# Kernel tuning notes

Measured on AMD Instinct MI355X. Metric: run time of the kernel, lower is better.

Reference implementation:

```python
import jax, jax.numpy as jnp
import numpy as np
from jax import lax

D_MODEL = 1024
D_STATE = 16
D_CONV = 4
EXPAND = 2
D_INNER = EXPAND * D_MODEL
LN_EPS = 1e-5


def setup_inputs() -> dict:
    key = jax.random.key(0)
    ks = jax.random.split(key, 12)
    B, L = 4, 1024
    s = lambda fan_in: 1.0 / np.sqrt(fan_in)
    inp = {
        "x": jax.random.normal(ks[0], (B, L, D_MODEL), jnp.float32),
        # in_proj: d_model -> 2*d_inner (stored as (in, out))
        "W_in": jax.random.normal(ks[1], (D_MODEL, 2 * D_INNER), jnp.float32) * s(D_MODEL),
        "b_in": jnp.zeros((2 * D_INNER,), jnp.float32),
        # depthwise causal conv1d, kernel (d_inner, 1, d_conv)
        "conv_w": jax.random.normal(ks[2], (D_INNER, 1, D_CONV), jnp.float32) * s(D_CONV),
        "conv_b": jnp.zeros((D_INNER,), jnp.float32),
        # x_proj: d_inner -> 2*d_state
        "W_xp": jax.random.normal(ks[3], (D_INNER, 2 * D_STATE), jnp.float32) * s(D_INNER),
        "b_xp": jnp.zeros((2 * D_STATE,), jnp.float32),
        # dt_proj: d_inner -> d_inner
        "W_dt": jax.random.normal(ks[4], (D_INNER, D_INNER), jnp.float32) * s(D_INNER),
        "b_dt": jnp.zeros((D_INNER,), jnp.float32),
        # A_log = log(arange(1, d_state+1)) repeated over d_inner
        "A_log": jnp.log(jnp.broadcast_to(jnp.arange(1, D_STATE + 1, dtype=jnp.float32), (D_INNER, D_STATE))),
        "D_param": jnp.ones((D_INNER,), jnp.float32),
        # out_proj: d_inner -> d_model
        "W_out": jax.random.normal(ks[5], (D_INNER, D_MODEL), jnp.float32) * s(D_INNER),
        "b_out": jnp.zeros((D_MODEL,), jnp.float32),
        "ln_g": jnp.ones((D_MODEL,), jnp.float32),
        "ln_b": jnp.zeros((D_MODEL,), jnp.float32),
    }
    return inp


def _causal_depthwise_conv(x, w, b):
    # x: (B, d_inner, L); w: (d_inner, 1, d_conv). Left-pad d_conv-1 => causal.
    y = lax.conv_general_dilated(
        x, w, window_strides=(1,), padding=[(D_CONV - 1, 0)],
        dimension_numbers=("NCH", "OIH", "NCH"), feature_group_count=D_INNER)
    return y + b[None, :, None]


def _ssm(x, A, Bm, Cm, dt, D_param):
    # x, dt: (B,L,D)  A: (D,N)  Bm, Cm: (B,L,N)
    A_disc = jnp.exp(dt[..., None] * A)               # (B,L,D,N)
    dBx = (dt * x)[..., None] * Bm[:, :, None, :]     # (B,L,D,N) = dt*B*x_t
    h0 = jnp.zeros(x.shape[:1] + A.shape, x.dtype)    # (B,D,N)

    def step(h, inputs):
        a, bx, c = inputs                              # (B,D,N),(B,D,N),(B,N)
        h = a * h + bx
        y = jnp.einsum("bdn,bn->bd", h, c)
        return h, y

    _, ys = lax.scan(step, h0, (jnp.swapaxes(A_disc, 0, 1),
                                jnp.swapaxes(dBx, 0, 1),
                                jnp.swapaxes(Cm, 0, 1)))
    y = jnp.swapaxes(ys, 0, 1)                         # (B,L,D)
    return y + x * D_param


def reference(x, W_in, b_in, conv_w, conv_b, W_xp, b_xp, W_dt, b_dt,
              A_log, D_param, W_out, b_out, ln_g, ln_b):
    residual = x
    xr = x @ W_in + b_in                               # (B,L,2*d_inner)
    xi, res = jnp.split(xr, 2, axis=-1)
    xi = jax.nn.silu(xi)
    xi = jnp.swapaxes(xi, 1, 2)                        # (B,d_inner,L)
    xi = _causal_depthwise_conv(xi, conv_w, conv_b)
    xi = jnp.swapaxes(xi, 1, 2)
    xi = jax.nn.silu(xi)
    bc = xi @ W_xp + b_xp                              # (B,L,2*d_state)
    Bm, Cm = jnp.split(bc, 2, axis=-1)
    dt = jax.nn.softplus(xi @ W_dt + b_dt)
    A = -jnp.exp(A_log)                                # (d_inner, d_state)
    y = _ssm(xi, A, Bm, Cm, dt, D_param)
    y = y * jax.nn.silu(res)
    out = y @ W_out + b_out
    z = out + residual
    mu = jnp.mean(z, axis=-1, keepdims=True)
    var = jnp.var(z, axis=-1, keepdims=True)
    return (z - mu) * jax.lax.rsqrt(var + LN_EPS) * ln_g + ln_b
```

## Files before the change

kernel.cpp:

```cpp
#include <hip/hip_runtime.h>
#include <math.h>

#define D_MODEL 1024
#define D_INNER 2048
#define D_STATE 16
#define D_CONV  4
#define NCHUNK  8
#define LCHUNK  128

typedef unsigned short u16;
typedef __attribute__((ext_vector_type(8))) short short8;
typedef __attribute__((ext_vector_type(4))) float f32x4;
typedef __attribute__((ext_vector_type(4))) unsigned short u16x4;

__device__ __forceinline__ float silu_f(float x) { return x / (1.f + __expf(-x)); }
__device__ __forceinline__ float softplus_f(float x) {
    return fmaxf(x, 0.f) + log1pf(__expf(-fabsf(x)));
}
__device__ __forceinline__ u16 f2bf(float f) {
    union { float f; unsigned u; } c; c.f = f;
    unsigned r = c.u + 0x7fffu + ((c.u >> 16) & 1u);
    return (u16)(r >> 16);
}
__device__ __forceinline__ float bf2f(u16 v) {
    union { unsigned u; float f; } c; c.u = ((unsigned)v) << 16; return c.f;
}
__device__ __forceinline__ void gload_lds16(const void* g, void* l) {
    __builtin_amdgcn_global_load_lds((const __attribute__((address_space(1))) void*)g,
                                     (__attribute__((address_space(3))) void*)l, 16, 0, 0);
}

__global__ __launch_bounds__(256)
void f32_to_bf16_kernel(const float* __restrict__ in, u16* __restrict__ out, int n4)
{
    const int i = blockIdx.x * 256 + threadIdx.x;
    if (i >= n4) return;
    const float4 v = *(const float4*)&in[(size_t)i * 4];
    u16x4 o; o.x = f2bf(v.x); o.y = f2bf(v.y); o.z = f2bf(v.z); o.w = f2bf(v.w);
    *(u16x4*)&out[(size_t)i * 4] = o;
}

__global__ __launch_bounds__(256)
void transpose_bf16_kernel(const float* __restrict__ W, u16* __restrict__ Wt, int K, int N)
{
    __shared__ float tile[32][33];
    const int tx = threadIdx.x & 31, ty = threadIdx.x >> 5;
    const int n0 = blockIdx.x * 32, k0 = blockIdx.y * 32;
#pragma unroll
    for (int q = 0; q < 4; q++)
        tile[ty + q * 8][tx] = W[(size_t)(k0 + ty + q * 8) * N + n0 + tx];
    __syncthreads();
#pragma unroll
    for (int q = 0; q < 4; q++)
        Wt[(size_t)(n0 + ty + q * 8) * K + k0 + tx] = f2bf(tile[tx][ty + q * 8]);
}

template <int MODE>
__global__ __launch_bounds__(256)
void gemm_mfma(const u16* __restrict__ A, const u16* __restrict__ Bt,
               const float* __restrict__ bias, const float* __restrict__ aux,
               void* __restrict__ out0v, void* __restrict__ out1v,
               int M, int N, int K)
{
    __shared__ __align__(16) short As[3][4096];
    __shared__ __align__(16) short Bs[3][4096];

    const int tid = threadIdx.x;
    const int wid = tid >> 6, lane = tid & 63;
    const int wr = wid >> 1, wc = wid & 1;
    const int row0 = blockIdx.y * 128, col0 = blockIdx.x * 128;

    f32x4 acc[4][4] = {};

    const int c0 = wid * 128 + lane;
    const int c1 = c0 + 64;
    const u16* Abase = A + (size_t)row0 * K;
    const u16* Bbase = Bt + (size_t)col0 * K;

    const int gsl8 = (((lane & 3) ^ ((lane >> 3) & 3)) << 3);

    const int kg = lane >> 4, r16 = lane & 15;
    const int sl8 = ((kg ^ ((r16 >> 1) & 3)) << 3);

#define STAGE(bi, kk) do {                                                                   \
        gload_lds16(Abase + (size_t)(c0 >> 2) * K + (kk) + gsl8, &As[bi][wid * 1024]);       \
        gload_lds16(Abase + (size_t)(c1 >> 2) * K + (kk) + gsl8, &As[bi][wid * 1024 + 512]); \
        gload_lds16(Bbase + (size_t)(c0 >> 2) * K + (kk) + gsl8, &Bs[bi][wid * 1024]);       \
        gload_lds16(Bbase + (size_t)(c1 >> 2) * K + (kk) + gsl8, &Bs[bi][wid * 1024 + 512]); \
    } while (0)

    const int nt = K >> 5;
    STAGE(0, 0);
    STAGE(1, 32);
    int cs = 0;
    for (int t = 0; t < nt; ++t) {
        if (t + 2 < nt) {
            const int ss = (cs + 2 >= 3) ? cs - 1 : cs + 2;
            STAGE(ss, (t + 2) << 5);
            asm volatile("s_waitcnt vmcnt(8)" ::: "memory");
        } else if (t + 1 < nt) {
            asm volatile("s_waitcnt vmcnt(4)" ::: "memory");
        } else {
            asm volatile("s_waitcnt vmcnt(0)" ::: "memory");
        }
        __builtin_amdgcn_s_barrier();

        short8 af[4], bg[4];
#pragma unroll
        for (int i = 0; i < 4; i++) {
            const int r = wr * 64 + i * 16 + r16;
            af[i] = *(const short8*)&As[cs][r * 32 + sl8];
        }
#pragma unroll
        for (int j = 0; j < 4; j++) {
            const int r = wc * 64 + j * 16 + r16;
            bg[j] = *(const short8*)&Bs[cs][r * 32 + sl8];
        }
        __builtin_amdgcn_s_setprio(1);
#pragma unroll
        for (int i = 0; i < 4; i++)
#pragma unroll
            for (int j = 0; j < 4; j++)
                acc[i][j] = __builtin_amdgcn_mfma_f32_16x16x32_bf16(af[i], bg[j], acc[i][j], 0, 0, 0);
        __builtin_amdgcn_s_setprio(0);

        asm volatile("s_waitcnt lgkmcnt(0)" ::: "memory");
        __builtin_amdgcn_s_barrier();
        cs = (cs + 1 >= 3) ? 0 : cs + 1;
    }
#undef STAGE

#pragma unroll
    for (int i = 0; i < 4; i++) {
#pragma unroll
        for (int j = 0; j < 4; j++) {
#pragma unroll
            for (int r = 0; r < 4; r++) {
                const int row = row0 + wr * 64 + i * 16 + kg * 4 + r;
                const int col = col0 + wc * 64 + j * 16 + r16;
                float v = acc[i][j][r] + bias[col];
                if (MODE == 0) {
                    u16* o0 = (u16*)out0v; u16* o1 = (u16*)out1v;
                    if (col < D_INNER) o0[(size_t)row * D_INNER + col] = f2bf(silu_f(v));
                    else               o1[(size_t)row * D_INNER + (col - D_INNER)] = f2bf(v);
                } else if (MODE == 1) {
                    ((float*)out0v)[(size_t)row * N + col] = softplus_f(v);
                } else {
                    ((float*)out0v)[(size_t)row * N + col] = v + aux[(size_t)row * N + col];
                }
            }
        }
    }
}

__global__ __launch_bounds__(256)
void conv_silu_kernel(const u16* __restrict__ xi, const float* __restrict__ w,
                      const float* __restrict__ cb, float* __restrict__ xc,
                      u16* __restrict__ xcb, int total)
{
    const int i = blockIdx.x * 256 + threadIdx.x;
    if (i >= total) return;
    const int d = i & (D_INNER - 1);
    const int l = (i >> 11) & 1023;
    float acc = cb[d];
#pragma unroll
    for (int k = 0; k < D_CONV; k++) {
        const int li = l + k - (D_CONV - 1);
        if (li >= 0) acc = fmaf(w[d * D_CONV + k], bf2f(xi[(size_t)i + (k - (D_CONV - 1)) * D_INNER]), acc);
    }
    const float s = silu_f(acc);
    xc[i] = s;
    xcb[i] = f2bf(s);
}

__global__ __launch_bounds__(256)
void xproj_mfma_kernel(const u16* __restrict__ A, const u16* __restrict__ Wt,
                       const float* __restrict__ bxp, float* __restrict__ bc)
{
    const int wid = threadIdx.x >> 6, lane = threadIdx.x & 63;
    const int kg = lane >> 4, r16 = lane & 15;
    const int tok0 = blockIdx.x * 64 + wid * 16;

    f32x4 acc[2] = {};
#pragma unroll 4
    for (int k0 = 0; k0 < D_INNER; k0 += 32) {
        const short8 a  = *(const short8*)&A[(size_t)(tok0 + r16) * D_INNER + k0 + kg * 8];
        const short8 b0 = *(const short8*)&Wt[(size_t)r16 * D_INNER + k0 + kg * 8];
        const short8 b1 = *(const short8*)&Wt[(size_t)(16 + r16) * D_INNER + k0 + kg * 8];
        acc[0] = __builtin_amdgcn_mfma_f32_16x16x32_bf16(a, b0, acc[0], 0, 0, 0);
        acc[1] = __builtin_amdgcn_mfma_f32_16x16x32_bf16(a, b1, acc[1], 0, 0, 0);
    }
#pragma unroll
    for (int j = 0; j < 2; j++)
#pragma unroll
        for (int r = 0; r < 4; r++) {
            const int token = tok0 + kg * 4 + r;
            const int c = j * 16 + r16;
            bc[(size_t)token * 32 + c] = acc[j][r] + bxp[c];
        }
}

__global__ __launch_bounds__(256)
void ssm_s1_kernel(const float* __restrict__ xc, const float* __restrict__ dt,
                   const float* __restrict__ bc, const float* __restrict__ A_log,
                   float* __restrict__ hend, float* __restrict__ dtsum)
{
    const int tid = threadIdx.x;
    const int ch = tid >> 4, n = tid & 15;
    const int d0 = blockIdx.x * 16;
    const int c = blockIdx.y;
    const int b = blockIdx.z;
    const int d = d0 + ch;

    const float Aln = -__expf(A_log[d * D_STATE + n]);

    __shared__ float sdt[64][16], sdtx[64][16], sB[64][16];

    float h = 0.f, S = 0.f;

    for (int half = 0; half < 2; half++) {
        const int l0 = c * LCHUNK + half * 64;
        __syncthreads();
        {
            const int l = tid >> 2, di = (tid & 3) << 2;
            const size_t g = ((size_t)(b * 1024 + l0 + l)) * D_INNER + d0 + di;
            const float4 dv = *(const float4*)&dt[g];
            const float4 xv = *(const float4*)&xc[g];
            float4 dx;
            dx.x = dv.x * xv.x; dx.y = dv.y * xv.y; dx.z = dv.z * xv.z; dx.w = dv.w * xv.w;
            *(float4*)&sdt[l][di] = dv;
            *(float4*)&sdtx[l][di] = dx;
            *(float4*)&sB[l][di] = *(const float4*)&bc[((size_t)(b * 1024 + l0 + l)) * 32 + di];
        }
        __syncthreads();
#pragma unroll 16
        for (int l = 0; l < 64; l++) {
            const float dtv = sdt[l][ch];
            const float a = __expf(dtv * Aln);
            h = fmaf(a, h, sdtx[l][ch] * sB[l][n]);
            S += dtv;
        }
    }
    hend[((size_t)(b * NCHUNK + c) * D_INNER + d) * D_STATE + n] = h;
    if (n == 0) dtsum[(size_t)(b * NCHUNK + c) * D_INNER + d] = S;
}

__global__ __launch_bounds__(256)
void ssm_s3_kernel(const float* __restrict__ xc, const float* __restrict__ dt,
                   const float* __restrict__ bc, const float* __restrict__ A_log,
                   const float* __restrict__ Dp, const u16* __restrict__ resbf,
                   const float* __restrict__ hend, const float* __restrict__ dtsum,
                   u16* __restrict__ ybf)
{
    const int tid = threadIdx.x;
    const int wid = tid >> 6, lane = tid & 63;
    const int ch4 = lane >> 4, n = lane & 15;
    const int ch = wid * 4 + ch4;
    const int d0 = blockIdx.x * 16;
    const int c = blockIdx.y;
    const int b = blockIdx.z;
    const int d = d0 + ch;

    const float Aln = -__expf(A_log[d * D_STATE + n]);
    const float Dv = Dp[d];

    float h = 0.f;
    for (int cc = 0; cc < c; cc++) {
        const float S = dtsum[(size_t)(b * NCHUNK + cc) * D_INNER + d];
        const float P = __expf(Aln * S);
        h = fmaf(P, h, hend[((size_t)(b * NCHUNK + cc) * D_INNER + d) * D_STATE + n]);
    }

    __shared__ float sdt[64][16], sdtx[64][16], sx[64][16], sres[64][16];
    __shared__ float sbc[64][32];
    __shared__ float pbuf[4 * 16 * 68];

    float* pw = &pbuf[wid * 16 * 68];

    for (int half = 0; half < 2; half++) {
        const int l0 = c * LCHUNK + half * 64;
        __syncthreads();
        {
            const int l = tid >> 2, di = (tid & 3) << 2;
            const size_t g = ((size_t)(b * 1024 + l0 + l)) * D_INNER + d0 + di;
            const float4 dv = *(const float4*)&dt[g];
            const float4 xv = *(const float4*)&xc[g];
            const u16x4 rv = *(const u16x4*)&resbf[g];
            float4 dx;
            dx.x = dv.x * xv.x; dx.y = dv.y * xv.y; dx.z = dv.z * xv.z; dx.w = dv.w * xv.w;
            *(float4*)&sdt[l][di] = dv;
            *(float4*)&sdtx[l][di] = dx;
            *(float4*)&sx[l][di] = xv;
            sres[l][di + 0] = bf2f(rv.x);
            sres[l][di + 1] = bf2f(rv.y);
            sres[l][di + 2] = bf2f(rv.z);
            sres[l][di + 3] = bf2f(rv.w);
            const int r0 = tid >> 3, c4 = (tid & 7) << 2;
            *(float4*)&sbc[r0][c4] = *(const float4*)&bc[((size_t)(b * 1024 + l0 + r0)) * 32 + c4];
            const int r1 = (tid + 256) >> 3;
            *(float4*)&sbc[r1][c4] = *(const float4*)&bc[((size_t)(b * 1024 + l0 + r1)) * 32 + c4];
        }
        __syncthreads();

        for (int l16 = 0; l16 < 4; l16++) {
#pragma unroll
            for (int j = 0; j < 16; j++) {
                const int l = l16 * 16 + j;
                const float dtv = sdt[l][ch];
                const float a = __expf(dtv * Aln);
                h = fmaf(a, h, sdtx[l][ch] * sbc[l][n]);
                pw[j * 68 + ch4 * 16 + n] = h * sbc[l][16 + n];
            }
            __builtin_amdgcn_wave_barrier();
            const float4 q0 = *(const float4*)&pw[n * 68 + ch4 * 16 + 0];
            const float4 q1 = *(const float4*)&pw[n * 68 + ch4 * 16 + 4];
            const float4 q2 = *(const float4*)&pw[n * 68 + ch4 * 16 + 8];
            const float4 q3 = *(const float4*)&pw[n * 68 + ch4 * 16 + 12];
            const float sum = ((q0.x + q0.y) + (q0.z + q0.w)) + ((q1.x + q1.y) + (q1.z + q1.w))
                            + ((q2.x + q2.y) + (q2.z + q2.w)) + ((q3.x + q3.y) + (q3.z + q3.w));
            const int t = l16 * 16 + n;
            const float xv = sx[t][ch];
            const float rv = sres[t][ch];
            const float yv = (sum + xv * Dv) * silu_f(rv);
            ybf[((size_t)(b * 1024 + l0 + t)) * D_INNER + d] = f2bf(yv);
            __builtin_amdgcn_wave_barrier();
        }
    }
}

__global__ __launch_bounds__(256)
void layernorm_kernel(const float* __restrict__ z, const float* __restrict__ g,
                      const float* __restrict__ beta, float* __restrict__ out)
{
    const int row = blockIdx.x;
    const int tid = threadIdx.x;
    const float* zr = z + (size_t)row * D_MODEL;
    const float4 v = *(const float4*)&zr[tid << 2];
    float s = v.x + v.y + v.z + v.w;
    float ss = v.x * v.x + v.y * v.y + v.z * v.z + v.w * v.w;

    __shared__ float sm[256], sq[256];
    sm[tid] = s; sq[tid] = ss;
    __syncthreads();
    for (int off = 128; off > 0; off >>= 1) {
        if (tid < off) { sm[tid] += sm[tid + off]; sq[tid] += sq[tid + off]; }
        __syncthreads();
    }
    const float mean = sm[0] * (1.f / D_MODEL);
    const float var = sq[0] * (1.f / D_MODEL) - mean * mean;
    const float rstd = rsqrtf(var + 1e-5f);

    float4 o;
    o.x = (v.x - mean) * rstd * g[(tid << 2) + 0] + beta[(tid << 2) + 0];
    o.y = (v.y - mean) * rstd * g[(tid << 2) + 1] + beta[(tid << 2) + 1];
    o.z = (v.z - mean) * rstd * g[(tid << 2) + 2] + beta[(tid << 2) + 2];
    o.w = (v.w - mean) * rstd * g[(tid << 2) + 3] + beta[(tid << 2) + 3];
    *(float4*)&out[(size_t)row * D_MODEL + (tid << 2)] = o;
}

extern "C" void kernel_launch(void* const* d_in, const int* in_sizes, int n_in,
                              void* d_out, int out_size, void* d_ws, size_t ws_size,
                              hipStream_t stream)
{
    const float* x      = (const float*)d_in[0];
    const float* W_in   = (const float*)d_in[1];
    const float* b_in   = (const float*)d_in[2];
    const float* conv_w = (const float*)d_in[3];
    const float* conv_b = (const float*)d_in[4];
    const float* W_xp   = (const float*)d_in[5];
    const float* b_xp   = (const float*)d_in[6];
    const float* W_dt   = (const float*)d_in[7];
    const float* b_dt   = (const float*)d_in[8];
    const float* A_log  = (const float*)d_in[9];
    const float* D_par  = (const float*)d_in[10];
    const float* W_out  = (const float*)d_in[11];
    const float* b_out  = (const float*)d_in[12];
    const float* ln_g   = (const float*)d_in[13];
    const float* ln_b   = (const float*)d_in[14];
    float* out = (float*)d_out;

    const int BL = in_sizes[0] / D_MODEL;
    const int Bb = BL / 1024;
    const size_t BLD = (size_t)BL * D_INNER;

    float* ws    = (float*)d_ws;
    float* xcb   = ws;
    float* dtb   = xcb + BLD;
    float* bcbuf = dtb + BLD;
    float* hend  = bcbuf + (size_t)BL * 32;
    float* dtsum = hend + (size_t)Bb * NCHUNK * D_INNER * D_STATE;
    u16*   xibf  = (u16*)(dtsum + (size_t)Bb * NCHUNK * D_INNER);
    u16*   resbf = xibf + BLD;
    u16*   xcbf  = resbf + BLD;
    u16*   xbf   = xcbf + BLD;
    u16*   wxpT  = xbf + (size_t)BL * D_MODEL;
    u16*   wtmp  = wxpT + 32 * D_INNER;
    u16*   ybf   = xibf;
    float* zbuf  = dtb;

    f32_to_bf16_kernel<<<(BL * D_MODEL / 4 + 255) / 256, 256, 0, stream>>>(x, xbf, BL * D_MODEL / 4);

    transpose_bf16_kernel<<<dim3(2 * D_INNER / 32, D_MODEL / 32), 256, 0, stream>>>(W_in, wtmp, D_MODEL, 2 * D_INNER);

    gemm_mfma<0><<<dim3(2 * D_INNER / 128, BL / 128), 256, 0, stream>>>(
        xbf, wtmp, b_in, nullptr, xibf, resbf, BL, 2 * D_INNER, D_MODEL);

    transpose_bf16_kernel<<<dim3(1, D_INNER / 32), 256, 0, stream>>>(W_xp, wxpT, D_INNER, 32);

    conv_silu_kernel<<<(int)(BLD / 256), 256, 0, stream>>>(
        xibf, conv_w, conv_b, xcb, xcbf, (int)BLD);

    xproj_mfma_kernel<<<BL / 64, 256, 0, stream>>>(xcbf, wxpT, b_xp, bcbuf);

    transpose_bf16_kernel<<<dim3(D_INNER / 32, D_INNER / 32), 256, 0, stream>>>(W_dt, wtmp, D_INNER, D_INNER);

    gemm_mfma<1><<<dim3(D_INNER / 128, BL / 128), 256, 0, stream>>>(
        xcbf, wtmp, b_dt, nullptr, dtb, nullptr, BL, D_INNER, D_INNER);

    ssm_s1_kernel<<<dim3(D_INNER / 16, NCHUNK, Bb), 256, 0, stream>>>(
        xcb, dtb, bcbuf, A_log, hend, dtsum);

    ssm_s3_kernel<<<dim3(D_INNER / 16, NCHUNK, Bb), 256, 0, stream>>>(
        xcb, dtb, bcbuf, A_log, D_par, resbf, hend, dtsum, ybf);

    transpose_bf16_kernel<<<dim3(D_MODEL / 32, D_INNER / 32), 256, 0, stream>>>(W_out, wtmp, D_INNER, D_MODEL);

    gemm_mfma<2><<<dim3(D_MODEL / 128, BL / 128), 256, 0, stream>>>(
        ybf, wtmp, b_out, x, zbuf, nullptr, BL, D_MODEL, D_INNER);

    layernorm_kernel<<<BL, 256, 0, stream>>>(zbuf, ln_g, ln_b, out);
}
```

Baseline: 368.2 us.

## Use 256x256 GEMM tiles for in/dt projections and halve SSM chunk length

Adds a 512-thread GEMM kernel with 256x256 output tiles, a K-step of 64 and double-buffered LDS, and uses it for the in_proj and dt_proj GEMMs. The larger tile raises arithmetic intensity and cuts global reloads. It also halves the SSM chunk length to 64 with twice as many chunks, removing the inner half loop and doubling the parallel blocks in the scan kernels. The risks are fewer blocks per GEMM, which hurts occupancy and wave balance, and a longer cross-chunk combine.

```diff
diff --git a/kernel.cpp b/kernel.cpp
--- a/kernel.cpp
+++ b/kernel.cpp
@@ -5,8 +5,8 @@
 #define D_INNER 2048
 #define D_STATE 16
 #define D_CONV  4
-#define NCHUNK  8
-#define LCHUNK  128
+#define NCHUNK  16
+#define LCHUNK  64
 
 typedef unsigned short u16;
 typedef __attribute__((ext_vector_type(8))) short short8;
@@ -56,11 +56,103 @@
 }
 
 template <int MODE>
-__global__ __launch_bounds__(256)
-void gemm_mfma(const u16* __restrict__ A, const u16* __restrict__ Bt,
-               const float* __restrict__ bias, const float* __restrict__ aux,
-               void* __restrict__ out0v, void* __restrict__ out1v,
-               int M, int N, int K)
+__global__ __launch_bounds__(512, 2)
+void gemm_mfma256(const u16* __restrict__ A, const u16* __restrict__ Bt,
+                  const float* __restrict__ bias,
+                  void* __restrict__ out0v, void* __restrict__ out1v,
+                  int M, int N, int K)
+{
+    __shared__ __align__(16) short As[2][256 * 64];
+    __shared__ __align__(16) short Bs[2][256 * 64];
+
+    const int tid = threadIdx.x;
+    const int wid = tid >> 6, lane = tid & 63;
+    const int wr = wid >> 2, wc = wid & 3;
+    const int row0 = blockIdx.y * 256, col0 = blockIdx.x * 256;
+    const int kg = lane >> 4, r16 = lane & 15;
+
+    f32x4 acc[8][4] = {};
+
+    const u16* Abase = A + (size_t)row0 * K;
+    const u16* Bbase = Bt + (size_t)col0 * K;
+
+#define STAGE256(bi, kk) do {                                                   \
+        _Pragma("unroll")                                                       \
+        for (int q = 0; q < 4; q++) {                                           \
+            const int c = (q << 9) + tid;                                       \
+            const int r = c >> 3;                                               \
+            const int ks8 = (((c & 7) ^ (r & 7)) << 3);                         \
+            gload_lds16(Abase + (size_t)r * K + (kk) + ks8,                     \
+                        &As[bi][(((q << 9) + (wid << 6))) << 3]);               \
+            gload_lds16(Bbase + (size_t)r * K + (kk) + ks8,                     \
+                        &Bs[bi][(((q << 9) + (wid << 6))) << 3]);               \
+        }                                                                       \
+    } while (0)
+
+    const int nt = K >> 6;
+    STAGE256(0, 0);
+    asm volatile("s_waitcnt vmcnt(0)" ::: "memory");
+    __builtin_amdgcn_s_barrier();
+
+    int cur = 0;
+    for (int t = 0; t < nt; ++t) {
+        if (t + 1 < nt) STAGE256(cur ^ 1, (t + 1) << 6);
+
+        const int rx = r16 & 7;
+#pragma unroll
+        for (int ks = 0; ks < 2; ks++) {
+            const int sl8 = (((ks << 2) + kg) ^ rx) << 3;
+            short8 af[8], bg[4];
+#pragma unroll
+            for (int i = 0; i < 8; i++) {
+                const int r = wr * 128 + i * 16 + r16;
+                af[i] = *(const short8*)&As[cur][r * 64 + sl8];
+            }
+#pragma unroll
+            for (int j = 0; j < 4; j++) {
+                const int r = wc * 64 + j * 16 + r16;
+                bg[j] = *(const short8*)&Bs[cur][r * 64 + sl8];
+            }
+            __builtin_amdgcn_s_setprio(1);
+#pragma unroll
+            for (int i = 0; i < 8; i++)
+#pragma unroll
+                for (int j = 0; j < 4; j++)
+                    acc[i][j] = __builtin_amdgcn_mfma_f32_16x16x32_bf16(af[i], bg[j], acc[i][j], 0, 0, 0);
+            __builtin_amdgcn_s_setprio(0);
+        }
+
+        asm volatile("s_waitcnt vmcnt(0)" ::: "memory");
+        __builtin_amdgcn_s_barrier();
+        cur ^= 1;
+    }
+#undef STAGE256
+
+#pragma unroll
+    for (int i = 0; i < 8; i++) {
+#pragma unroll
+        for (int j = 0; j < 4; j++) {
+#pragma unroll
+            for (int r = 0; r < 4; r++) {
+                const int row = row0 + wr * 128 + i * 16 + kg * 4 + r;
+                const int col = col0 + wc * 64 + j * 16 + r16;
+                float v = acc[i][j][r] + bias[col];
+                if (MODE == 0) {
+                    u16* o0 = (u16*)out0v; u16* o1 = (u16*)out1v;
+                    if (col < D_INNER) o0[(size_t)row * D_INNER + col] = f2bf(silu_f(v));
+                    else               o1[(size_t)row * D_INNER + (col - D_INNER)] = f2bf(v);
+                } else {
+                    ((float*)out0v)[(size_t)row * N + col] = softplus_f(v);
+                }
+            }
+        }
+    }
+}
+
+__global__ __launch_bounds__(256)
+void gemm_mfma_128(const u16* __restrict__ A, const u16* __restrict__ Bt,
+                   const float* __restrict__ bias, const float* __restrict__ aux,
+                   float* __restrict__ out0, int M, int N, int K)
 {
     __shared__ __align__(16) short As[3][4096];
     __shared__ __align__(16) short Bs[3][4096];
@@ -78,7 +170,6 @@
     const u16* Bbase = Bt + (size_t)col0 * K;
 
     const int gsl8 = (((lane & 3) ^ ((lane >> 3) & 3)) << 3);
-
     const int kg = lane >> 4, r16 = lane & 15;
     const int sl8 = ((kg ^ ((r16 >> 1) & 3)) << 3);
 
@@ -139,15 +230,7 @@
                 const int row = row0 + wr * 64 + i * 16 + kg * 4 + r;
                 const int col = col0 + wc * 64 + j * 16 + r16;
                 float v = acc[i][j][r] + bias[col];
-                if (MODE == 0) {
-                    u16* o0 = (u16*)out0v; u16* o1 = (u16*)out1v;
-                    if (col < D_INNER) o0[(size_t)row * D_INNER + col] = f2bf(silu_f(v));
-                    else               o1[(size_t)row * D_INNER + (col - D_INNER)] = f2bf(v);
-                } else if (MODE == 1) {
-                    ((float*)out0v)[(size_t)row * N + col] = softplus_f(v);
-                } else {
-                    ((float*)out0v)[(size_t)row * N + col] = v + aux[(size_t)row * N + col];
-                }
+                out0[(size_t)row * N + col] = v + aux[(size_t)row * N + col];
             }
         }
     }
@@ -218,28 +301,25 @@
 
     float h = 0.f, S = 0.f;
 
-    for (int half = 0; half < 2; half++) {
-        const int l0 = c * LCHUNK + half * 64;
-        __syncthreads();
-        {
-            const int l = tid >> 2, di = (tid & 3) << 2;
-            const size_t g = ((size_t)(b * 1024 + l0 + l)) * D_INNER + d0 + di;
-            const float4 dv = *(const float4*)&dt[g];
-            const float4 xv = *(const float4*)&xc[g];
-            float4 dx;
-            dx.x = dv.x * xv.x; dx.y = dv.y * xv.y; dx.z = dv.z * xv.z; dx.w = dv.w * xv.w;
-            *(float4*)&sdt[l][di] = dv;
-            *(float4*)&sdtx[l][di] = dx;
-            *(float4*)&sB[l][di] = *(const float4*)&bc[((size_t)(b * 1024 + l0 + l)) * 32 + di];
-        }
-        __syncthreads();
+    const int l0 = c * LCHUNK;
+    {
+        const int l = tid >> 2, di = (tid & 3) << 2;
+        const size_t g = ((size_t)(b * 1024 + l0 + l)) * D_INNER + d0 + di;
+        const float4 dv = *(const float4*)&dt[g];
+        const float4 xv = *(const float4*)&xc[g];
+        float4 dx;
+        dx.x = dv.x * xv.x; dx.y = dv.y * xv.y; dx.z = dv.z * xv.z; dx.w = dv.w * xv.w;
+        *(float4*)&sdt[l][di] = dv;
+        *(float4*)&sdtx[l][di] = dx;
+        *(float4*)&sB[l][di] = *(const float4*)&bc[((size_t)(b * 1024 + l0 + l)) * 32 + di];
+    }
+    __syncthreads();
 #pragma unroll 16
-        for (int l = 0; l < 64; l++) {
-            const float dtv = sdt[l][ch];
-            const float a = __expf(dtv * Aln);
-            h = fmaf(a, h, sdtx[l][ch] * sB[l][n]);
-            S += dtv;
-        }
+    for (int l = 0; l < 64; l++) {
+        const float dtv = sdt[l][ch];
+        const float a = __expf(dtv * Aln);
+        h = fmaf(a, h, sdtx[l][ch] * sB[l][n]);
+        S += dtv;
     }
     hend[((size_t)(b * NCHUNK + c) * D_INNER + d) * D_STATE + n] = h;
     if (n == 0) dtsum[(size_t)(b * NCHUNK + c) * D_INNER + d] = S;
@@ -277,54 +357,51 @@
 
     float* pw = &pbuf[wid * 16 * 68];
 
-    for (int half = 0; half < 2; half++) {
-        const int l0 = c * LCHUNK + half * 64;
-        __syncthreads();
-        {
-            const int l = tid >> 2, di = (tid & 3) << 2;
-            const size_t g = ((size_t)(b * 1024 + l0 + l)) * D_INNER + d0 + di;
-            const float4 dv = *(const float4*)&dt[g];
-            const float4 xv = *(const float4*)&xc[g];
-            const u16x4 rv = *(const u16x4*)&resbf[g];
-            float4 dx;
-            dx.x = dv.x * xv.x; dx.y = dv.y * xv.y; dx.z = dv.z * xv.z; dx.w = dv.w * xv.w;
-            *(float4*)&sdt[l][di] = dv;
-            *(float4*)&sdtx[l][di] = dx;
-            *(float4*)&sx[l][di] = xv;
-            sres[l][di + 0] = bf2f(rv.x);
-            sres[l][di + 1] = bf2f(rv.y);
-            sres[l][di + 2] = bf2f(rv.z);
-            sres[l][di + 3] = bf2f(rv.w);
-            const int r0 = tid >> 3, c4 = (tid & 7) << 2;
-            *(float4*)&sbc[r0][c4] = *(const float4*)&bc[((size_t)(b * 1024 + l0 + r0)) * 32 + c4];
-            const int r1 = (tid + 256) >> 3;
-            *(float4*)&sbc[r1][c4] = *(const float4*)&bc[((size_t)(b * 1024 + l0 + r1)) * 32 + c4];
-        }
-        __syncthreads();
-
-        for (int l16 = 0; l16 < 4; l16++) {
-#pragma unroll
-            for (int j = 0; j < 16; j++) {
-                const int l = l16 * 16 + j;
-                const float dtv = sdt[l][ch];
-                const float a = __expf(dtv * Aln);
-                h = fmaf(a, h, sdtx[l][ch] * sbc[l][n]);
-                pw[j * 68 + ch4 * 16 + n] = h * sbc[l][16 + n];
-            }
-            __builtin_amdgcn_wave_barrier();
-            const float4 q0 = *(const float4*)&pw[n * 68 + ch4 * 16 + 0];
-            const float4 q1 = *(const float4*)&pw[n * 68 + ch4 * 16 + 4];
-            const float4 q2 = *(const float4*)&pw[n * 68 + ch4 * 16 + 8];
-            const float4 q3 = *(const float4*)&pw[n * 68 + ch4 * 16 + 12];
-            const float sum = ((q0.x + q0.y) + (q0.z + q0.w)) + ((q1.x + q1.y) + (q1.z + q1.w))
-                            + ((q2.x + q2.y) + (q2.z + q2.w)) + ((q3.x + q3.y) + (q3.z + q3.w));
-            const int t = l16 * 16 + n;
-            const float xv = sx[t][ch];
-            const float rv = sres[t][ch];
-            const float yv = (sum + xv * Dv) * silu_f(rv);
-            ybf[((size_t)(b * 1024 + l0 + t)) * D_INNER + d] = f2bf(yv);
-            __builtin_amdgcn_wave_barrier();
-        }
+    const int l0 = c * LCHUNK;
+    {
+        const int l = tid >> 2, di = (tid & 3) << 2;
+        const size_t g = ((size_t)(b * 1024 + l0 + l)) * D_INNER + d0 + di;
+        const float4 dv = *(const float4*)&dt[g];
+        const float4 xv = *(const float4*)&xc[g];
+        const u16x4 rv = *(const u16x4*)&resbf[g];
+        float4 dx;
+        dx.x = dv.x * xv.x; dx.y = dv.y * xv.y; dx.z = dv.z * xv.z; dx.w = dv.w * xv.w;
+        *(float4*)&sdt[l][di] = dv;
+        *(float4*)&sdtx[l][di] = dx;
+        *(float4*)&sx[l][di] = xv;
+        sres[l][di + 0] = bf2f(rv.x);
+        sres[l][di + 1] = bf2f(rv.y);
+        sres[l][di + 2] = bf2f(rv.z);
+        sres[l][di + 3] = bf2f(rv.w);
+        const int r0 = tid >> 3, c4 = (tid & 7) << 2;
+        *(float4*)&sbc[r0][c4] = *(const float4*)&bc[((size_t)(b * 1024 + l0 + r0)) * 32 + c4];
+        const int r1 = (tid + 256) >> 3;
+        *(float4*)&sbc[r1][c4] = *(const float4*)&bc[((size_t)(b * 1024 + l0 + r1)) * 32 + c4];
+    }
+    __syncthreads();
+
+    for (int l16 = 0; l16 < 4; l16++) {
+#pragma unroll
+        for (int j = 0; j < 16; j++) {
+            const int l = l16 * 16 + j;
+            const float dtv = sdt[l][ch];
+            const float a = __expf(dtv * Aln);
+            h = fmaf(a, h, sdtx[l][ch] * sbc[l][n]);
+            pw[j * 68 + ch4 * 16 + n] = h * sbc[l][16 + n];
+        }
+        __builtin_amdgcn_wave_barrier();
+        const float4 q0 = *(const float4*)&pw[n * 68 + ch4 * 16 + 0];
+        const float4 q1 = *(const float4*)&pw[n * 68 + ch4 * 16 + 4];
+        const float4 q2 = *(const float4*)&pw[n * 68 + ch4 * 16 + 8];
+        const float4 q3 = *(const float4*)&pw[n * 68 + ch4 * 16 + 12];
+        const float sum = ((q0.x + q0.y) + (q0.z + q0.w)) + ((q1.x + q1.y) + (q1.z + q1.w))
+                        + ((q2.x + q2.y) + (q2.z + q2.w)) + ((q3.x + q3.y) + (q3.z + q3.w));
+        const int t = l16 * 16 + n;
+        const float xv = sx[t][ch];
+        const float rv = sres[t][ch];
+        const float yv = (sum + xv * Dv) * silu_f(rv);
+        ybf[((size_t)(b * 1024 + l0 + t)) * D_INNER + d] = f2bf(yv);
+        __builtin_amdgcn_wave_barrier();
     }
 }
 
@@ -402,8 +479,8 @@
 
     transpose_bf16_kernel<<<dim3(2 * D_INNER / 32, D_MODEL / 32), 256, 0, stream>>>(W_in, wtmp, D_MODEL, 2 * D_INNER);
 
-    gemm_mfma<0><<<dim3(2 * D_INNER / 128, BL / 128), 256, 0, stream>>>(
-        xbf, wtmp, b_in, nullptr, xibf, resbf, BL, 2 * D_INNER, D_MODEL);
+    gemm_mfma256<0><<<dim3(2 * D_INNER / 256, BL / 256), 512, 0, stream>>>(
+        xbf, wtmp, b_in, xibf, resbf, BL, 2 * D_INNER, D_MODEL);
 
     transpose_bf16_kernel<<<dim3(1, D_INNER / 32), 256, 0, stream>>>(W_xp, wxpT, D_INNER, 32);
 
@@ -414,8 +491,8 @@
 
     transpose_bf16_kernel<<<dim3(D_INNER / 32, D_INNER / 32), 256, 0, stream>>>(W_dt, wtmp, D_INNER, D_INNER);
 
-    gemm_mfma<1><<<dim3(D_INNER / 128, BL / 128), 256, 0, stream>>>(
-        xcbf, wtmp, b_dt, nullptr, dtb, nullptr, BL, D_INNER, D_INNER);
+    gemm_mfma256<1><<<dim3(D_INNER / 256, BL / 256), 512, 0, stream>>>(
+        xcbf, wtmp, b_dt, dtb, nullptr, BL, D_INNER, D_INNER);
 
     ssm_s1_kernel<<<dim3(D_INNER / 16, NCHUNK, Bb), 256, 0, stream>>>(
         xcb, dtb, bcbuf, A_log, hend, dtsum);
@@ -425,8 +502,8 @@
 
     transpose_bf16_kernel<<<dim3(D_MODEL / 32, D_INNER / 32), 256, 0, stream>>>(W_out, wtmp, D_INNER, D_MODEL);
 
-    gemm_mfma<2><<<dim3(D_MODEL / 128, BL / 128), 256, 0, stream>>>(
-        ybf, wtmp, b_out, x, zbuf, nullptr, BL, D_MODEL, D_INNER);
+    gemm_mfma_128<<<dim3(D_MODEL / 128, BL / 128), 256, 0, stream>>>(
+        ybf, wtmp, b_out, x, zbuf, BL, D_MODEL, D_INNER);
 
     layernorm_kernel<<<BL, 256, 0, stream>>>(zbuf, ln_g, ln_b, out);
 }
```

After: 396.8 us. 7.8% more time.
